# Performance work log

Measured on AMD Instinct MI355X. Metric: run time of the kernel, lower is better.

The kernel has to match this reference:

```python
import jax, jax.numpy as jnp
import numpy as np

B, N, G = 16, 6000, 512
NUM_PAD_GT = 64  # zero-padded gt rows per image


def _make_boxes(key, shape):
    # sample two corner points and sort so (y1,x1) <= (y2,x2)
    r = jax.random.uniform(key, shape[:-1] + (4,), dtype=jnp.float32)
    lo = jnp.minimum(r[..., :2], r[..., 2:])
    hi = jnp.maximum(r[..., :2], r[..., 2:])
    return jnp.concatenate([lo, hi], axis=-1)


def setup_inputs() -> dict:
    key = jax.random.key(0)
    k1, k2, k3 = jax.random.split(key, 3)
    rois = _make_boxes(k1, (B, N, 4))
    gt_boxes = _make_boxes(k2, (B, G, 4))
    # zero-pad tail gt rows (remove_zero_padding signal)
    gt_boxes = gt_boxes.at[:, G - NUM_PAD_GT:, :].set(0.0)
    # ids in [-2, 18]: <0 crowd, ==0 padding, >0 real classes
    gt_ids = jax.random.randint(k3, (B, G), 0, 21, dtype=jnp.int64) - 2
    gt_ids = jnp.where(jnp.arange(G) >= G - NUM_PAD_GT, 0, gt_ids)
    return {"rois": rois, "gt_ids": gt_ids, "gt_boxes": gt_boxes}


def _pairwise_iou(boxes1, boxes2):
    # boxes1: [B,N,4], boxes2: [B,G,4] in (y1,x1,y2,x2) -> IoU [B,N,G]
    b1 = boxes1[:, :, None, :]  # [B,N,1,4]
    b2 = boxes2[:, None, :, :]  # [B,1,G,4]
    y1 = jnp.maximum(b1[..., 0], b2[..., 0])
    x1 = jnp.maximum(b1[..., 1], b2[..., 1])
    y2 = jnp.minimum(b1[..., 2], b2[..., 2])
    x2 = jnp.minimum(b1[..., 3], b2[..., 3])
    inter = jnp.maximum(y2 - y1, 0.0) * jnp.maximum(x2 - x1, 0.0)
    area1 = (b1[..., 2] - b1[..., 0]) * (b1[..., 3] - b1[..., 1])
    area2 = (b2[..., 2] - b2[..., 0]) * (b2[..., 3] - b2[..., 1])
    union = area1 + area2 - inter
    return inter / (union + 1e-8)


def reference(rois, gt_ids, gt_boxes):
    # remove_zero_padding -> validity masks (jit-friendly: mask instead of gather)
    valid_roi = jnp.sum(jnp.abs(rois), axis=-1) > 0.0      # [B,N]
    valid_gt = jnp.sum(jnp.abs(gt_boxes), axis=-1) > 0.0   # [B,G]
    crowd = valid_gt & (gt_ids < 0)                          # [B,G]
    non_crowd = valid_gt & (gt_ids > 0)                      # [B,G]

    iou = _pairwise_iou(rois, gt_boxes)                      # [B,N,G]
    # max IoU against non-crowd / crowd gt subsets (masked cols -> 0, IoU >= 0)
    iou_nc_max = jnp.max(jnp.where(non_crowd[:, None, :], iou, 0.0), axis=2)
    iou_c_max = jnp.max(jnp.where(crowd[:, None, :], iou, 0.0), axis=2)
    iou_nc_max = jnp.where(valid_roi, iou_nc_max, 0.0)       # [B,N]
    iou_c_max = jnp.where(valid_roi, iou_c_max, 0.0)

    positive_mask = valid_roi & (iou_nc_max >= 0.5)
    negative_mask = valid_roi & (iou_nc_max < 0.5) & (iou_c_max < 1e-3)

    iou_maxes = jnp.stack([iou_nc_max, iou_c_max], axis=1)   # [B,2,N]
    return iou_maxes, positive_mask, negative_mask
```

## Files before the change

### kernel.cpp

```cpp
#include <hip/hip_runtime.h>

#define BB 16
#define NN 6000
#define GG 512

__global__ __launch_bounds__(256) void det_assign_kernel(
    const float4* __restrict__ rois,
    const int*    __restrict__ gt_ids,
    const float4* __restrict__ gt_boxes,
    float*        __restrict__ out)
{
    __shared__ float4 s_box[GG];
    __shared__ float4 s_area4[GG / 4];
    __shared__ float  s_ncm[4][64];
    __shared__ float  s_cm[4][64];
    __shared__ int    s_cnt[2];
    float* s_area = (float*)s_area4;

    const int b    = blockIdx.y;
    const int tid  = threadIdx.x;
    const int wave = tid >> 6;
    const int lane = tid & 63;

    if (tid == 0) { s_cnt[0] = 0; s_cnt[1] = 0; }
    __syncthreads();

    for (int g = tid; g < GG; g += 256) {
        float4 box = gt_boxes[b * GG + g];
        float asum = fabsf(box.x) + fabsf(box.y) + fabsf(box.z) + fabsf(box.w);
        int id = gt_ids[b * GG + g];
        if (asum > 0.0f && id != 0) {
            int idx;
            if (id > 0) idx = atomicAdd(&s_cnt[0], 1);
            else        idx = (GG - 1) - atomicAdd(&s_cnt[1], 1);
            s_box[idx]  = box;
            s_area[idx] = (box.z - box.x) * (box.w - box.y);
        }
    }
    __syncthreads();

    const int n = blockIdx.x * 64 + lane;
    const float4 r = (n < NN) ? rois[b * NN + n] : make_float4(0.f, 0.f, 0.f, 0.f);
    const bool vroi = (fabsf(r.x) + fabsf(r.y) + fabsf(r.z) + fabsf(r.w)) > 0.0f;
    const float rsum = (r.z - r.x) * (r.w - r.y) + 1e-8f;

    const int ncnt = __builtin_amdgcn_readfirstlane(s_cnt[0]);
    const int ccnt = __builtin_amdgcn_readfirstlane(s_cnt[1]);

    auto iou_of = [&](float4 gb, float ga) -> float {
        float yy1 = fmaxf(r.x, gb.x);
        float xx1 = fmaxf(r.y, gb.y);
        float yy2 = fminf(r.z, gb.z);
        float xx2 = fminf(r.w, gb.w);
        float inter = fmaxf(yy2 - yy1, 0.0f) * fmaxf(xx2 - xx1, 0.0f);
        float uni = rsum + ga - inter;
        return inter * __builtin_amdgcn_rcpf(uni);
    };

    float ncm = 0.0f;
    {
        const int chunk = (((ncnt + 3) >> 2) + 3) & ~3;
        const int g0 = wave * chunk;
        const int g1 = min(ncnt, g0 + chunk);
        int g = g0;
        for (; g + 4 <= g1; g += 4) {
            float4 b0 = s_box[g + 0];
            float4 b1 = s_box[g + 1];
            float4 b2 = s_box[g + 2];
            float4 b3 = s_box[g + 3];
            float4 a4 = s_area4[g >> 2];
            float i0 = iou_of(b0, a4.x);
            float i1 = iou_of(b1, a4.y);
            float i2 = iou_of(b2, a4.z);
            float i3 = iou_of(b3, a4.w);
            ncm = fmaxf(ncm, fmaxf(fmaxf(i0, i1), fmaxf(i2, i3)));
        }
        for (; g < g1; ++g) ncm = fmaxf(ncm, iou_of(s_box[g], s_area[g]));
    }

    float cm = 0.0f;
    {
        const int chunkc = (((ccnt + 3) >> 2) + 3) & ~3;
        const int hi = GG - wave * chunkc;
        const int lo = max(GG - ccnt, hi - chunkc);
        int g = hi;
        while (g - 4 >= lo) {
            g -= 4;
            float4 b0 = s_box[g + 0];
            float4 b1 = s_box[g + 1];
            float4 b2 = s_box[g + 2];
            float4 b3 = s_box[g + 3];
            float4 a4 = s_area4[g >> 2];
            float i0 = iou_of(b0, a4.x);
            float i1 = iou_of(b1, a4.y);
            float i2 = iou_of(b2, a4.z);
            float i3 = iou_of(b3, a4.w);
            cm = fmaxf(cm, fmaxf(fmaxf(i0, i1), fmaxf(i2, i3)));
        }
        while (g > lo) { --g; cm = fmaxf(cm, iou_of(s_box[g], s_area[g])); }
    }

    s_ncm[wave][lane] = ncm;
    s_cm[wave][lane]  = cm;
    __syncthreads();

    if (wave == 0 && n < NN) {
        float a = fmaxf(fmaxf(s_ncm[0][lane], s_ncm[1][lane]),
                        fmaxf(s_ncm[2][lane], s_ncm[3][lane]));
        float c = fmaxf(fmaxf(s_cm[0][lane], s_cm[1][lane]),
                        fmaxf(s_cm[2][lane], s_cm[3][lane]));
        const float nc_max = vroi ? a : 0.0f;
        const float c_max  = vroi ? c : 0.0f;

        out[b * 2 * NN + n]      = nc_max;
        out[b * 2 * NN + NN + n] = c_max;
        const float pos = (vroi && nc_max >= 0.5f) ? 1.0f : 0.0f;
        const float neg = (vroi && nc_max < 0.5f && c_max < 0.001f) ? 1.0f : 0.0f;
        out[BB * 2 * NN + b * NN + n]           = pos;
        out[BB * 2 * NN + BB * NN + b * NN + n] = neg;
    }
}

extern "C" void kernel_launch(void* const* d_in, const int* in_sizes, int n_in,
                              void* d_out, int out_size, void* d_ws, size_t ws_size,
                              hipStream_t stream) {
    const float4* rois     = (const float4*)d_in[0];
    const int*    gt_ids   = (const int*)d_in[1];
    const float4* gt_boxes = (const float4*)d_in[2];
    float*        out      = (float*)d_out;

    dim3 grid((NN + 63) / 64, BB);
    det_assign_kernel<<<grid, 256, 0, stream>>>(rois, gt_ids, gt_boxes, out);
}
```

Baseline: 27.06 us.

## Split gt compaction into a separate kernel and widen main blocks to 8 waves

Ground-truth filtering and compaction now runs once per image in a small pre-kernel that writes compacted boxes, areas and counts to workspace. The main kernel only copies those into shared memory, so the 94 blocks per image no longer each redo the atomics and scans. The main kernel also uses 8 waves per block instead of 4, which halves the gt range each wave covers. The cost is a second kernel launch and a serial dependency, plus larger blocks that may lower occupancy. A fallback single-kernel path is kept for when workspace is too small.

```diff
diff --git a/kernel.cpp b/kernel.cpp
--- a/kernel.cpp
+++ b/kernel.cpp
@@ -4,24 +4,21 @@
 #define NN 6000
 #define GG 512
 
-__global__ __launch_bounds__(256) void det_assign_kernel(
-    const float4* __restrict__ rois,
+#define WS_BOX_OFF   0
+#define WS_AREA_OFF  (BB * GG * 16)
+#define WS_CNT_OFF   (BB * GG * 20)
+#define WS_NEEDED    (WS_CNT_OFF + BB * 8)
+
+__global__ __launch_bounds__(256) void compact_kernel(
     const int*    __restrict__ gt_ids,
     const float4* __restrict__ gt_boxes,
-    float*        __restrict__ out)
+    float4*       __restrict__ ws_box,
+    float*        __restrict__ ws_area,
+    int*          __restrict__ ws_cnt)
 {
-    __shared__ float4 s_box[GG];
-    __shared__ float4 s_area4[GG / 4];
-    __shared__ float  s_ncm[4][64];
-    __shared__ float  s_cm[4][64];
-    __shared__ int    s_cnt[2];
-    float* s_area = (float*)s_area4;
-
-    const int b    = blockIdx.y;
-    const int tid  = threadIdx.x;
-    const int wave = tid >> 6;
-    const int lane = tid & 63;
-
+    __shared__ int s_cnt[2];
+    const int b   = blockIdx.x;
+    const int tid = threadIdx.x;
     if (tid == 0) { s_cnt[0] = 0; s_cnt[1] = 0; }
     __syncthreads();
 
@@ -33,19 +30,44 @@
             int idx;
             if (id > 0) idx = atomicAdd(&s_cnt[0], 1);
             else        idx = (GG - 1) - atomicAdd(&s_cnt[1], 1);
-            s_box[idx]  = box;
-            s_area[idx] = (box.z - box.x) * (box.w - box.y);
-        }
-    }
-    __syncthreads();
+            ws_box[b * GG + idx]  = box;
+            ws_area[b * GG + idx] = (box.z - box.x) * (box.w - box.y);
+        }
+    }
+    __syncthreads();
+    if (tid == 0) { ws_cnt[b * 2 + 0] = s_cnt[0]; ws_cnt[b * 2 + 1] = s_cnt[1]; }
+}
+
+#define WAVES 8
+__global__ __launch_bounds__(64 * WAVES) void det_main_kernel(
+    const float4* __restrict__ rois,
+    const float4* __restrict__ ws_box,
+    const float4* __restrict__ ws_area4,
+    const int*    __restrict__ ws_cnt,
+    float*        __restrict__ out)
+{
+    __shared__ float4 s_box[GG];
+    __shared__ float4 s_area4[GG / 4];
+    __shared__ float  s_ncm[WAVES][64];
+    __shared__ float  s_cm[WAVES][64];
+    float* s_area = (float*)s_area4;
+
+    const int b    = blockIdx.y;
+    const int tid  = threadIdx.x;
+    const int wave = tid >> 6;
+    const int lane = tid & 63;
+
+    for (int i = tid; i < GG; i += 64 * WAVES)     s_box[i]   = ws_box[b * GG + i];
+    for (int i = tid; i < GG / 4; i += 64 * WAVES) s_area4[i] = ws_area4[b * (GG / 4) + i];
+    __syncthreads();
+
+    const int ncnt = ws_cnt[b * 2 + 0];
+    const int ccnt = ws_cnt[b * 2 + 1];
 
     const int n = blockIdx.x * 64 + lane;
     const float4 r = (n < NN) ? rois[b * NN + n] : make_float4(0.f, 0.f, 0.f, 0.f);
     const bool vroi = (fabsf(r.x) + fabsf(r.y) + fabsf(r.z) + fabsf(r.w)) > 0.0f;
     const float rsum = (r.z - r.x) * (r.w - r.y) + 1e-8f;
-
-    const int ncnt = __builtin_amdgcn_readfirstlane(s_cnt[0]);
-    const int ccnt = __builtin_amdgcn_readfirstlane(s_cnt[1]);
 
     auto iou_of = [&](float4 gb, float ga) -> float {
         float yy1 = fmaxf(r.x, gb.x);
@@ -59,7 +81,7 @@
 
     float ncm = 0.0f;
     {
-        const int chunk = (((ncnt + 3) >> 2) + 3) & ~3;
+        const int chunk = ((((ncnt + WAVES - 1) / WAVES) + 3) & ~3);
         const int g0 = wave * chunk;
         const int g1 = min(ncnt, g0 + chunk);
         int g = g0;
@@ -80,7 +102,7 @@
 
     float cm = 0.0f;
     {
-        const int chunkc = (((ccnt + 3) >> 2) + 3) & ~3;
+        const int chunkc = ((((ccnt + WAVES - 1) / WAVES) + 3) & ~3);
         const int hi = GG - wave * chunkc;
         const int lo = max(GG - ccnt, hi - chunkc);
         int g = hi;
@@ -105,13 +127,98 @@
     __syncthreads();
 
     if (wave == 0 && n < NN) {
+        float a = s_ncm[0][lane], c = s_cm[0][lane];
+        #pragma unroll
+        for (int w = 1; w < WAVES; ++w) {
+            a = fmaxf(a, s_ncm[w][lane]);
+            c = fmaxf(c, s_cm[w][lane]);
+        }
+        const float nc_max = vroi ? a : 0.0f;
+        const float c_max  = vroi ? c : 0.0f;
+
+        out[b * 2 * NN + n]      = nc_max;
+        out[b * 2 * NN + NN + n] = c_max;
+        const float pos = (vroi && nc_max >= 0.5f) ? 1.0f : 0.0f;
+        const float neg = (vroi && nc_max < 0.5f && c_max < 0.001f) ? 1.0f : 0.0f;
+        out[BB * 2 * NN + b * NN + n]           = pos;
+        out[BB * 2 * NN + BB * NN + b * NN + n] = neg;
+    }
+}
+
+__global__ __launch_bounds__(256) void det_assign_fallback(
+    const float4* __restrict__ rois,
+    const int*    __restrict__ gt_ids,
+    const float4* __restrict__ gt_boxes,
+    float*        __restrict__ out)
+{
+    __shared__ float4 s_box[GG];
+    __shared__ float4 s_area4[GG / 4];
+    __shared__ float  s_ncm[4][64];
+    __shared__ float  s_cm[4][64];
+    __shared__ int    s_cnt[2];
+    float* s_area = (float*)s_area4;
+
+    const int b    = blockIdx.y;
+    const int tid  = threadIdx.x;
+    const int wave = tid >> 6;
+    const int lane = tid & 63;
+
+    if (tid == 0) { s_cnt[0] = 0; s_cnt[1] = 0; }
+    __syncthreads();
+    for (int g = tid; g < GG; g += 256) {
+        float4 box = gt_boxes[b * GG + g];
+        float asum = fabsf(box.x) + fabsf(box.y) + fabsf(box.z) + fabsf(box.w);
+        int id = gt_ids[b * GG + g];
+        if (asum > 0.0f && id != 0) {
+            int idx;
+            if (id > 0) idx = atomicAdd(&s_cnt[0], 1);
+            else        idx = (GG - 1) - atomicAdd(&s_cnt[1], 1);
+            s_box[idx]  = box;
+            s_area[idx] = (box.z - box.x) * (box.w - box.y);
+        }
+    }
+    __syncthreads();
+
+    const int n = blockIdx.x * 64 + lane;
+    const float4 r = (n < NN) ? rois[b * NN + n] : make_float4(0.f, 0.f, 0.f, 0.f);
+    const bool vroi = (fabsf(r.x) + fabsf(r.y) + fabsf(r.z) + fabsf(r.w)) > 0.0f;
+    const float rsum = (r.z - r.x) * (r.w - r.y) + 1e-8f;
+    const int ncnt = __builtin_amdgcn_readfirstlane(s_cnt[0]);
+    const int ccnt = __builtin_amdgcn_readfirstlane(s_cnt[1]);
+
+    auto iou_of = [&](float4 gb, float ga) -> float {
+        float yy1 = fmaxf(r.x, gb.x);
+        float xx1 = fmaxf(r.y, gb.y);
+        float yy2 = fminf(r.z, gb.z);
+        float xx2 = fminf(r.w, gb.w);
+        float inter = fmaxf(yy2 - yy1, 0.0f) * fmaxf(xx2 - xx1, 0.0f);
+        return inter * __builtin_amdgcn_rcpf(rsum + ga - inter);
+    };
+
+    float ncm = 0.0f;
+    {
+        const int chunk = (((ncnt + 3) >> 2) + 3) & ~3;
+        const int g0 = wave * chunk;
+        const int g1 = min(ncnt, g0 + chunk);
+        for (int g = g0; g < g1; ++g) ncm = fmaxf(ncm, iou_of(s_box[g], s_area[g]));
+    }
+    float cm = 0.0f;
+    {
+        const int chunkc = (((ccnt + 3) >> 2) + 3) & ~3;
+        const int hi = GG - wave * chunkc;
+        const int lo = max(GG - ccnt, hi - chunkc);
+        for (int g = lo; g < hi; ++g) cm = fmaxf(cm, iou_of(s_box[g], s_area[g]));
+    }
+    s_ncm[wave][lane] = ncm;
+    s_cm[wave][lane]  = cm;
+    __syncthreads();
+    if (wave == 0 && n < NN) {
         float a = fmaxf(fmaxf(s_ncm[0][lane], s_ncm[1][lane]),
                         fmaxf(s_ncm[2][lane], s_ncm[3][lane]));
         float c = fmaxf(fmaxf(s_cm[0][lane], s_cm[1][lane]),
                         fmaxf(s_cm[2][lane], s_cm[3][lane]));
         const float nc_max = vroi ? a : 0.0f;
         const float c_max  = vroi ? c : 0.0f;
-
         out[b * 2 * NN + n]      = nc_max;
         out[b * 2 * NN + NN + n] = c_max;
         const float pos = (vroi && nc_max >= 0.5f) ? 1.0f : 0.0f;
@@ -129,6 +236,18 @@
     const float4* gt_boxes = (const float4*)d_in[2];
     float*        out      = (float*)d_out;
 
-    dim3 grid((NN + 63) / 64, BB);
-    det_assign_kernel<<<grid, 256, 0, stream>>>(rois, gt_ids, gt_boxes, out);
-}
+    if (ws_size >= (size_t)WS_NEEDED) {
+        char* ws = (char*)d_ws;
+        float4* ws_box   = (float4*)(ws + WS_BOX_OFF);
+        float*  ws_area  = (float*)(ws + WS_AREA_OFF);
+        int*    ws_cnt   = (int*)(ws + WS_CNT_OFF);
+
+        compact_kernel<<<BB, 256, 0, stream>>>(gt_ids, gt_boxes, ws_box, ws_area, ws_cnt);
+        dim3 grid((NN + 63) / 64, BB);
+        det_main_kernel<<<grid, 64 * WAVES, 0, stream>>>(
+            rois, ws_box, (const float4*)ws_area, ws_cnt, out);
+    } else {
+        dim3 grid((NN + 63) / 64, BB);
+        det_assign_fallback<<<grid, 256, 0, stream>>>(rois, gt_ids, gt_boxes, out);
+    }
+}
```

Result: slower. 30.79 us (+13.8%).
